# Kernel tuning notes

Hardware: AMD Instinct MI355X
Metric: run time of the kernel (lower is better)

Reference implementation:

```python
import jax, jax.numpy as jnp
import numpy as np

NEURONS = 4096
K = 512

def setup_inputs() -> dict:
    key = jax.random.key(0)
    s = jax.random.normal(key, (16384, NEURONS), dtype=jnp.float32)
    return {"s": s}

def reference(s) -> jnp.ndarray:
    # Original: sort each row ascending, zero the smallest (neurons - k) entries,
    # i.e. keep only the k largest values per row. With continuous random inputs
    # (no ties) this equals thresholding at the k-th largest value per row.
    topk_vals, _ = jax.lax.top_k(s, K)          # [B, K], descending
    thresh = topk_vals[:, -1:]                   # k-th largest per row, [B, 1]
    return jnp.where(s >= thresh, s, jnp.zeros((), dtype=s.dtype))
```

## Files before the change

### kernel.cpp

```cpp
#include <hip/hip_runtime.h>

#define ROWS 16384
#define COLS 4096
#define KSEL 512
#define THREADS 256

__device__ __forceinline__ unsigned map_f(float f) {
    unsigned u = __float_as_uint(f);
    return (u & 0x80000000u) ? ~u : (u | 0x80000000u);
}

__device__ __forceinline__ float unmap_f(unsigned u) {
    unsigned b = (u & 0x80000000u) ? (u & 0x7FFFFFFFu) : ~u;
    return __uint_as_float(b);
}

__global__ __launch_bounds__(THREADS) void kwta_kernel(const float* __restrict__ in,
                                                       float* __restrict__ out) {
    __shared__ unsigned hist[256];
    __shared__ unsigned scan[256];
    __shared__ unsigned sh_prefix;
    __shared__ unsigned sh_k;

    const int row = blockIdx.x;
    const int t = threadIdx.x;
    const float4* __restrict__ inrow  = (const float4*)(in  + (size_t)row * COLS);
    float4* __restrict__ outrow       = (float4*)(out + (size_t)row * COLS);

    float4 f[4];
#pragma unroll
    for (int i = 0; i < 4; i++) f[i] = inrow[t + i * THREADS];

    unsigned v[16];
#pragma unroll
    for (int i = 0; i < 4; i++) {
        v[4 * i + 0] = map_f(f[i].x);
        v[4 * i + 1] = map_f(f[i].y);
        v[4 * i + 2] = map_f(f[i].z);
        v[4 * i + 3] = map_f(f[i].w);
    }

    unsigned prefix = 0;
    unsigned kk = KSEL;

#pragma unroll
    for (int pass = 0; pass < 4; pass++) {
        const int shift = 24 - 8 * pass;

        hist[t] = 0;
        __syncthreads();

        const unsigned pmask = (pass == 0) ? 0u : (0xFFFFFFFFu << (shift + 8));
#pragma unroll
        for (int i = 0; i < 16; i++) {
            if (pass == 0 || ((v[i] ^ prefix) & pmask) == 0u) {
                atomicAdd(&hist[(v[i] >> shift) & 255u], 1u);
            }
        }
        __syncthreads();

        scan[t] = hist[t];
        __syncthreads();
#pragma unroll
        for (int off = 1; off < 256; off <<= 1) {
            unsigned add = (t + off < 256) ? scan[t + off] : 0u;
            __syncthreads();
            scan[t] += add;
            __syncthreads();
        }
        const unsigned S       = scan[t];
        const unsigned S_above = (t == 255) ? 0u : scan[t + 1];

        if (S >= kk && S_above < kk) {
            sh_prefix = prefix | ((unsigned)t << shift);
            sh_k      = kk - S_above;
        }
        __syncthreads();
        prefix = sh_prefix;
        kk     = sh_k;
        __syncthreads();
    }

    const float thresh = unmap_f(prefix);

#pragma unroll
    for (int i = 0; i < 4; i++) {
        float4 o;
        o.x = (f[i].x >= thresh) ? f[i].x : 0.0f;
        o.y = (f[i].y >= thresh) ? f[i].y : 0.0f;
        o.z = (f[i].z >= thresh) ? f[i].z : 0.0f;
        o.w = (f[i].w >= thresh) ? f[i].w : 0.0f;
        outrow[t + i * THREADS] = o;
    }
}

extern "C" void kernel_launch(void* const* d_in, const int* in_sizes, int n_in,
                              void* d_out, int out_size, void* d_ws, size_t ws_size,
                              hipStream_t stream) {
    const float* s = (const float*)d_in[0];
    float* out = (float*)d_out;
    kwta_kernel<<<ROWS, THREADS, 0, stream>>>(s, out);
}
```

Measured before the change: 452.0 us.

## Process one row per wavefront with replicated LDS histograms and shuffle scan

Each 64-lane wavefront now handles a whole row, holding 64 values per lane in registers. Per-pass histograms are written to four LDS copies selected by lane to spread atomic contention. The block-wide scan with many __syncthreads is replaced by a wave shuffle scan plus a ballot to pick the threshold digit. Branchless float-to-key mapping and a comparison done on mapped keys remove the stored float copies. The costs are high register pressure (64 values per lane) and less parallelism per row.

```diff
diff --git a/kernel.cpp b/kernel.cpp
--- a/kernel.cpp
+++ b/kernel.cpp
@@ -3,41 +3,40 @@
 #define ROWS 16384
 #define COLS 4096
 #define KSEL 512
-#define THREADS 256
+#define WAVES_PER_BLOCK 4
+#define THREADS (WAVES_PER_BLOCK * 64)
+#define NCOPY 4
+#define HSTRIDE 260
 
 __device__ __forceinline__ unsigned map_f(float f) {
     unsigned u = __float_as_uint(f);
-    return (u & 0x80000000u) ? ~u : (u | 0x80000000u);
+    return u ^ (0x80000000u | (unsigned)((int)u >> 31));
+}
+__device__ __forceinline__ float unmap_f(unsigned m) {
+    return __uint_as_float(m ^ (0x80000000u | ~(unsigned)((int)m >> 31)));
 }
 
-__device__ __forceinline__ float unmap_f(unsigned u) {
-    unsigned b = (u & 0x80000000u) ? (u & 0x7FFFFFFFu) : ~u;
-    return __uint_as_float(b);
-}
+__global__ __launch_bounds__(THREADS, 4) void kwta_kernel(const float* __restrict__ in,
+                                                          float* __restrict__ out) {
+    __shared__ __align__(16) unsigned histmem[WAVES_PER_BLOCK][NCOPY * HSTRIDE];
 
-__global__ __launch_bounds__(THREADS) void kwta_kernel(const float* __restrict__ in,
-                                                       float* __restrict__ out) {
-    __shared__ unsigned hist[256];
-    __shared__ unsigned scan[256];
-    __shared__ unsigned sh_prefix;
-    __shared__ unsigned sh_k;
+    const int lane = threadIdx.x & 63;
+    const int wave = threadIdx.x >> 6;
+    const int row  = blockIdx.x * WAVES_PER_BLOCK + wave;
+    unsigned* h = histmem[wave];
+    const int copy = (lane & 3) * HSTRIDE;
 
-    const int row = blockIdx.x;
-    const int t = threadIdx.x;
     const float4* __restrict__ inrow  = (const float4*)(in  + (size_t)row * COLS);
-    float4* __restrict__ outrow       = (float4*)(out + (size_t)row * COLS);
+    float4*       __restrict__ outrow = (float4*)(out + (size_t)row * COLS);
 
-    float4 f[4];
+    unsigned v[64];
 #pragma unroll
-    for (int i = 0; i < 4; i++) f[i] = inrow[t + i * THREADS];
-
-    unsigned v[16];
-#pragma unroll
-    for (int i = 0; i < 4; i++) {
-        v[4 * i + 0] = map_f(f[i].x);
-        v[4 * i + 1] = map_f(f[i].y);
-        v[4 * i + 2] = map_f(f[i].z);
-        v[4 * i + 3] = map_f(f[i].w);
+    for (int i = 0; i < 16; i++) {
+        float4 f = inrow[lane + 64 * i];
+        v[4 * i + 0] = map_f(f.x);
+        v[4 * i + 1] = map_f(f.y);
+        v[4 * i + 2] = map_f(f.z);
+        v[4 * i + 3] = map_f(f.w);
     }
 
     unsigned prefix = 0;
@@ -47,50 +46,70 @@
     for (int pass = 0; pass < 4; pass++) {
         const int shift = 24 - 8 * pass;
 
-        hist[t] = 0;
-        __syncthreads();
+        uint4 z = make_uint4(0u, 0u, 0u, 0u);
+#pragma unroll
+        for (int i = 0; i < 5; i++) {
+            int w4 = lane + 64 * i;
+            if (w4 < (NCOPY * HSTRIDE) / 4) ((uint4*)h)[w4] = z;
+        }
 
-        const unsigned pmask = (pass == 0) ? 0u : (0xFFFFFFFFu << (shift + 8));
+        if (pass == 0) {
 #pragma unroll
-        for (int i = 0; i < 16; i++) {
-            if (pass == 0 || ((v[i] ^ prefix) & pmask) == 0u) {
-                atomicAdd(&hist[(v[i] >> shift) & 255u], 1u);
+            for (int i = 0; i < 64; i++)
+                atomicAdd(&h[copy + (v[i] >> 24)], 1u);
+        } else {
+            const int hs = shift + 8;
+#pragma unroll
+            for (int i = 0; i < 64; i++) {
+                if (((v[i] ^ prefix) >> hs) == 0u)
+                    atomicAdd(&h[copy + ((v[i] >> shift) & 255u)], 1u);
             }
         }
-        __syncthreads();
 
-        scan[t] = hist[t];
-        __syncthreads();
+        uint4 c0 = ((const uint4*)(h + 0 * HSTRIDE))[lane];
+        uint4 c1 = ((const uint4*)(h + 1 * HSTRIDE))[lane];
+        uint4 c2 = ((const uint4*)(h + 2 * HSTRIDE))[lane];
+        uint4 c3 = ((const uint4*)(h + 3 * HSTRIDE))[lane];
+        unsigned n0 = c0.x + c1.x + c2.x + c3.x;
+        unsigned n1 = c0.y + c1.y + c2.y + c3.y;
+        unsigned n2 = c0.z + c1.z + c2.z + c3.z;
+        unsigned n3 = c0.w + c1.w + c2.w + c3.w;
+
+        unsigned ls3 = n3, ls2 = n3 + n2, ls1 = ls2 + n1, tot = ls1 + n0;
+
+        unsigned S = tot;
 #pragma unroll
-        for (int off = 1; off < 256; off <<= 1) {
-            unsigned add = (t + off < 256) ? scan[t + off] : 0u;
-            __syncthreads();
-            scan[t] += add;
-            __syncthreads();
+        for (int off = 1; off < 64; off <<= 1) {
+            unsigned o = __shfl(S, lane + off);
+            S += (lane + off < 64) ? o : 0u;
         }
-        const unsigned S       = scan[t];
-        const unsigned S_above = (t == 255) ? 0u : scan[t + 1];
+        const unsigned R = S - tot;
 
-        if (S >= kk && S_above < kk) {
-            sh_prefix = prefix | ((unsigned)t << shift);
-            sh_k      = kk - S_above;
-        }
-        __syncthreads();
-        prefix = sh_prefix;
-        kk     = sh_k;
-        __syncthreads();
+        const unsigned S3 = R + ls3, S2 = R + ls2, S1 = R + ls1, S0 = R + tot;
+        unsigned dig = 0, nk = 0;
+        bool found = false;
+        if (S3 >= kk && R  < kk) { dig = 4 * lane + 3; nk = kk - R;  found = true; }
+        if (S2 >= kk && S3 < kk) { dig = 4 * lane + 2; nk = kk - S3; found = true; }
+        if (S1 >= kk && S2 < kk) { dig = 4 * lane + 1; nk = kk - S2; found = true; }
+        if (S0 >= kk && S1 < kk) { dig = 4 * lane + 0; nk = kk - S1; found = true; }
+
+        unsigned long long m = __ballot(found);
+        int src = (int)__ffsll((unsigned long long)m) - 1;
+        dig = __shfl(dig, src);
+        nk  = __shfl(nk, src);
+
+        prefix |= dig << shift;
+        kk = nk;
     }
 
-    const float thresh = unmap_f(prefix);
-
 #pragma unroll
-    for (int i = 0; i < 4; i++) {
+    for (int i = 0; i < 16; i++) {
         float4 o;
-        o.x = (f[i].x >= thresh) ? f[i].x : 0.0f;
-        o.y = (f[i].y >= thresh) ? f[i].y : 0.0f;
-        o.z = (f[i].z >= thresh) ? f[i].z : 0.0f;
-        o.w = (f[i].w >= thresh) ? f[i].w : 0.0f;
-        outrow[t + i * THREADS] = o;
+        o.x = (v[4 * i + 0] >= prefix) ? unmap_f(v[4 * i + 0]) : 0.0f;
+        o.y = (v[4 * i + 1] >= prefix) ? unmap_f(v[4 * i + 1]) : 0.0f;
+        o.z = (v[4 * i + 2] >= prefix) ? unmap_f(v[4 * i + 2]) : 0.0f;
+        o.w = (v[4 * i + 3] >= prefix) ? unmap_f(v[4 * i + 3]) : 0.0f;
+        outrow[lane + 64 * i] = o;
     }
 }
 
@@ -99,5 +118,5 @@
                               hipStream_t stream) {
     const float* s = (const float*)d_in[0];
     float* out = (float*)d_out;
-    kwta_kernel<<<ROWS, THREADS, 0, stream>>>(s, out);
+    kwta_kernel<<<ROWS / WAVES_PER_BLOCK, THREADS, 0, stream>>>(s, out);
 }
```

New measurement: 441.6 us. 2.3% less time.
